# Kernel tuning notes

Hardware: AMD Instinct MI355X
Metric: run time of the kernel (lower is better)

The kernel has to match this reference:

```python
import jax, jax.numpy as jnp
import numpy as np

NUM_NODE = 5000
EMBED_DIM = 256
NUM_CLS = 20
EDGE_ROWS = (NUM_NODE - 1) * (NUM_NODE - 1) + 1  # 24990002
BZ, SEQ, NBR = 64, 512, 16


def setup_inputs() -> dict:
    key = jax.random.key(0)
    k = jax.random.split(key, 8)
    X = jax.random.randint(k[0], (BZ, SEQ), 0, NUM_NODE)
    NX = jax.random.randint(k[1], (BZ, SEQ, NBR), 0, NUM_NODE)
    EW = jax.random.randint(k[2], (BZ, SEQ, NBR), 0, EDGE_ROWS)
    # parameters (xavier-ish scale); padding_idx=0 rows zeroed
    node_emb = jax.random.normal(k[3], (NUM_NODE, EMBED_DIM), jnp.float32) * 0.02
    node_emb = node_emb.at[0].set(0.0)
    edge_w = jax.random.normal(k[4], (EDGE_ROWS, 1), jnp.float32) * 0.02
    edge_w = edge_w.at[0].set(0.0)
    node_w = jax.random.normal(k[5], (NUM_NODE, 1), jnp.float32) * 0.02
    node_w = node_w.at[0].set(0.0)
    fc_W = jax.random.normal(k[6], (NUM_CLS, EMBED_DIM), jnp.float32) * 0.05
    fc_b = jnp.zeros((NUM_CLS,), jnp.float32)
    return {"X": X, "NX": NX, "EW": EW, "node_emb": node_emb,
            "edge_w": edge_w, "node_w": node_w, "fc_W": fc_W, "fc_b": fc_b}


def reference(X, NX, EW, node_emb, edge_w, node_w, fc_W, fc_b):
    Ra = node_emb[NX]                      # (bz, seq, nbr, d) neighbor embeddings
    Ean = edge_w[EW]                       # (bz, seq, nbr, 1) edge weights
    Mn = jnp.max(Ra * Ean, axis=2)         # (bz, seq, d) max over neighbors
    Rn = node_emb[X]                       # (bz, seq, d)
    Nn = node_w[X]                         # (bz, seq, 1)
    y = (1.0 - Nn) * Mn + Nn * Rn          # weighted combine
    y = jnp.sum(y, axis=1)                 # (bz, d) sum-pool over sequence
    y = y @ fc_W.T + fc_b                  # (bz, num_cls)
    y = jax.nn.relu(y)
    # Dropout is identity at inference; LogSoftmax over dim=1
    return jax.nn.log_softmax(y, axis=1)
```

## Files before the change

### kernel.cpp

```cpp
#include <hip/hip_runtime.h>
#include <math.h>

#define NUM_NODE 5000
#define BZ   64
#define SEQ  512
#define NBR  16
#define DIM  256
#define NCLS 20

#define ROWB  (DIM * 2)
#define NCHUNK2 (SEQ / 4)
#define NCHUNK16 (SEQ / 16)

__device__ __forceinline__ int bcast_i(int v, int lane) {
    return __builtin_amdgcn_readlane(v, lane);
}
__device__ __forceinline__ float bcast_f(float v, int lane) {
    return __int_as_float(__builtin_amdgcn_readlane(__float_as_int(v), lane));
}
__device__ __forceinline__ unsigned bf16_rne(float f) {
    unsigned u = __float_as_uint(f);
    return (u + 0x7fffu + ((u >> 16) & 1u)) >> 16;
}
__device__ __forceinline__ float lo_bf16(unsigned u) { return __uint_as_float(u << 16); }
__device__ __forceinline__ float hi_bf16(unsigned u) { return __uint_as_float(u & 0xffff0000u); }

__global__ __launch_bounds__(256) void zero_ws_kernel(float* __restrict__ ws, int n) {
    int i = blockIdx.x * blockDim.x + threadIdx.x;
    if (i < n) ws[i] = 0.0f;
}

__global__ __launch_bounds__(256) void cvt_emb_zero_kernel(
    const float4* __restrict__ src, uint2* __restrict__ dst, int n4,
    float* __restrict__ ypre, int nacc) {
    int i = blockIdx.x * blockDim.x + threadIdx.x;
    if (i < n4) {
        float4 v = src[i];
        uint2 o;
        o.x = bf16_rne(v.x) | (bf16_rne(v.y) << 16);
        o.y = bf16_rne(v.z) | (bf16_rne(v.w) << 16);
        dst[i] = o;
    }
    if (i < nacc) ypre[i] = 0.0f;
}

__global__ __launch_bounds__(256, 8) void gnn_gather_kernel(
    const int*   __restrict__ X,
    const int*   __restrict__ NX,
    const int*   __restrict__ EW,
    const char*  __restrict__ embb,
    const float* __restrict__ edge_w,
    const float* __restrict__ node_w,
    float*       __restrict__ ypre)
{
    __shared__ float lds[4][DIM];

    const int b     = blockIdx.x / NCHUNK2;
    const int chunk = blockIdx.x % NCHUNK2;
    const int wave  = threadIdx.x >> 6;
    const int lane  = threadIdx.x & 63;
    const int half  = lane >> 5;
    const int sub   = lane & 31;
    const int voff  = sub * 16;

    const int s  = chunk * 4 + wave;
    const int bs = b * SEQ + s;

    int   nxv = 0;
    float ewv = 0.f;
    if (lane < NBR) {
        nxv = __builtin_nontemporal_load(&NX[bs * NBR + lane]);
        const int ewi = __builtin_nontemporal_load(&EW[bs * NBR + lane]);
        ewv = __builtin_nontemporal_load(&edge_w[ewi]);
    }
    const int   x  = X[bs];
    const float nn = node_w[x];

    uint4 e[8];
    #pragma unroll
    for (int j = 0; j < 8; ++j) {
        const int n0 = bcast_i(nxv, 2 * j);
        const int n1 = bcast_i(nxv, 2 * j + 1);
        const int n  = half ? n1 : n0;
        e[j] = *(const uint4*)(embb + (size_t)n * ROWB + voff);
    }
    const uint4 es = *(const uint4*)(embb + (size_t)x * ROWB + voff);

    float m[8];
    #pragma unroll
    for (int i = 0; i < 8; ++i) m[i] = -INFINITY;

    #pragma unroll
    for (int j = 0; j < 8; ++j) {
        const float w0 = bcast_f(ewv, 2 * j);
        const float w1 = bcast_f(ewv, 2 * j + 1);
        const float w  = half ? w1 : w0;
        m[0] = fmaxf(m[0], lo_bf16(e[j].x) * w);
        m[1] = fmaxf(m[1], hi_bf16(e[j].x) * w);
        m[2] = fmaxf(m[2], lo_bf16(e[j].y) * w);
        m[3] = fmaxf(m[3], hi_bf16(e[j].y) * w);
        m[4] = fmaxf(m[4], lo_bf16(e[j].z) * w);
        m[5] = fmaxf(m[5], hi_bf16(e[j].z) * w);
        m[6] = fmaxf(m[6], lo_bf16(e[j].w) * w);
        m[7] = fmaxf(m[7], hi_bf16(e[j].w) * w);
    }

    #pragma unroll
    for (int i = 0; i < 8; ++i)
        m[i] = fmaxf(m[i], __shfl_xor(m[i], 32));

    const float om = 1.0f - nn;
    float acc[8];
    acc[0] = om * m[0] + nn * lo_bf16(es.x);
    acc[1] = om * m[1] + nn * hi_bf16(es.x);
    acc[2] = om * m[2] + nn * lo_bf16(es.y);
    acc[3] = om * m[3] + nn * hi_bf16(es.y);
    acc[4] = om * m[4] + nn * lo_bf16(es.z);
    acc[5] = om * m[5] + nn * hi_bf16(es.z);
    acc[6] = om * m[6] + nn * lo_bf16(es.w);
    acc[7] = om * m[7] + nn * hi_bf16(es.w);

    if (half == 0) {
        *(float4*)&lds[wave][8 * sub]     = make_float4(acc[0], acc[1], acc[2], acc[3]);
        *(float4*)&lds[wave][8 * sub + 4] = make_float4(acc[4], acc[5], acc[6], acc[7]);
    }
    __syncthreads();

    const int t = threadIdx.x;
    atomicAdd(&ypre[b * DIM + t], lds[0][t] + lds[1][t] + lds[2][t] + lds[3][t]);
}

__global__ __launch_bounds__(256) void gnn_gather_f32_kernel(
    const int*   __restrict__ X,
    const int*   __restrict__ NX,
    const int*   __restrict__ EW,
    const float* __restrict__ node_emb,
    const float* __restrict__ edge_w,
    const float* __restrict__ node_w,
    float*       __restrict__ dst)
{
    __shared__ float lds[4][DIM];
    const int b     = blockIdx.x / NCHUNK16;
    const int chunk = blockIdx.x % NCHUNK16;
    const int wave  = threadIdx.x >> 6;
    const int lane  = threadIdx.x & 63;
    const int s0  = chunk * 16 + wave * 4;
    const int bs0 = b * SEQ + s0;

    const int   nx  = NX[bs0 * NBR + lane];
    const float ew  = edge_w[EW[bs0 * NBR + lane]];
    int xv = 0; float nwv = 0.f;
    if (lane < 4) { xv = X[bs0 + lane]; nwv = node_w[xv]; }

    float4 acc = make_float4(0.f, 0.f, 0.f, 0.f);
    for (int p = 0; p < 4; ++p) {
        float4 m = make_float4(-INFINITY, -INFINITY, -INFINITY, -INFINITY);
        for (int k = 0; k < NBR; ++k) {
            const int   n = bcast_i(nx, p * 16 + k);
            const float w = bcast_f(ew, p * 16 + k);
            const float4 e = *(const float4*)(node_emb + (size_t)n * DIM + 4 * lane);
            m.x = fmaxf(m.x, e.x * w); m.y = fmaxf(m.y, e.y * w);
            m.z = fmaxf(m.z, e.z * w); m.w = fmaxf(m.w, e.w * w);
        }
        const int   x  = bcast_i(xv, p);
        const float nn = bcast_f(nwv, p);
        const float om = 1.0f - nn;
        const float4 r = *(const float4*)(node_emb + (size_t)x * DIM + 4 * lane);
        acc.x += om * m.x + nn * r.x; acc.y += om * m.y + nn * r.y;
        acc.z += om * m.z + nn * r.z; acc.w += om * m.w + nn * r.w;
    }
    *(float4*)&lds[wave][4 * lane] = acc;
    __syncthreads();
    const int t = threadIdx.x;
    atomicAdd(&dst[b * DIM + t], lds[0][t] + lds[1][t] + lds[2][t] + lds[3][t]);
}

__global__ __launch_bounds__(256) void gnn_head_kernel(
    const float* __restrict__ ypre,
    const float* __restrict__ fc_W,
    const float* __restrict__ fc_b,
    float*       __restrict__ out)
{
    __shared__ float vals[NCLS];
    __shared__ float lse;

    const int b = blockIdx.x;
    const int t = threadIdx.x;
    const int wave = t >> 6;
    const int lane = t & 63;

    const float4 y4 = *(const float4*)(ypre + b * DIM + 4 * lane);

    #pragma unroll
    for (int ci = 0; ci < 5; ++ci) {
        const int c = wave * 5 + ci;
        const float4 w4 = *(const float4*)(fc_W + c * DIM + 4 * lane);
        float d = y4.x * w4.x + y4.y * w4.y + y4.z * w4.z + y4.w * w4.w;
        #pragma unroll
        for (int off = 32; off; off >>= 1) d += __shfl_xor(d, off);
        if (lane == 0) vals[c] = fmaxf(d + fc_b[c], 0.0f);
    }
    __syncthreads();

    if (t == 0) {
        float mx = -INFINITY;
        for (int c = 0; c < NCLS; ++c) mx = fmaxf(mx, vals[c]);
        float s = 0.0f;
        for (int c = 0; c < NCLS; ++c) s += expf(vals[c] - mx);
        lse = mx + logf(s);
    }
    __syncthreads();

    if (t < NCLS) out[b * NCLS + t] = vals[t] - lse;
}

extern "C" void kernel_launch(void* const* d_in, const int* in_sizes, int n_in,
                              void* d_out, int out_size, void* d_ws, size_t ws_size,
                              hipStream_t stream) {
    const int*   X        = (const int*)  d_in[0];
    const int*   NX       = (const int*)  d_in[1];
    const int*   EW       = (const int*)  d_in[2];
    const float* node_emb = (const float*)d_in[3];
    const float* edge_w   = (const float*)d_in[4];
    const float* node_w   = (const float*)d_in[5];
    const float* fc_W     = (const float*)d_in[6];
    const float* fc_b     = (const float*)d_in[7];
    float* out = (float*)d_out;

    const size_t acc_bytes = (size_t)BZ * DIM * sizeof(float);
    const size_t emb_bytes = (size_t)NUM_NODE * DIM * sizeof(unsigned short);
    float* ypre = (float*)d_ws;
    char*  embb = (char*)d_ws + acc_bytes;

    if (ws_size >= acc_bytes + emb_bytes) {
        const int n4 = NUM_NODE * DIM / 4;
        cvt_emb_zero_kernel<<<(n4 + 255) / 256, 256, 0, stream>>>(
            (const float4*)node_emb, (uint2*)embb, n4, ypre, BZ * DIM);
        gnn_gather_kernel<<<BZ * NCHUNK2, 256, 0, stream>>>(
            X, NX, EW, embb, edge_w, node_w, ypre);
        gnn_head_kernel<<<BZ, 256, 0, stream>>>(ypre, fc_W, fc_b, out);
    } else {
        zero_ws_kernel<<<(BZ * DIM + 255) / 256, 256, 0, stream>>>(ypre, BZ * DIM);
        gnn_gather_f32_kernel<<<BZ * NCHUNK16, 256, 0, stream>>>(
            X, NX, EW, node_emb, edge_w, node_w, ypre);
        gnn_head_kernel<<<BZ, 256, 0, stream>>>(ypre, fc_W, fc_b, out);
    }
}
```

Baseline: 176.4 us.

## Process eight positions per wave with double-buffered neighbor embedding loads

Each wave now handles eight sequence positions instead of one, accumulating them in registers, so the grid shrinks eightfold and there are far fewer LDS reductions and global atomics. Embedding gathers for the next position are issued into a second register buffer while the current one is reduced, overlapping memory latency with compute. The cost is a higher register count, with the occupancy hint lowered from 8 to 4 blocks, and fewer blocks in flight to hide the latency of the random gathers.

Result: slower. 199.4 us (+13.1%).

```diff
diff --git a/kernel.cpp b/kernel.cpp
--- a/kernel.cpp
+++ b/kernel.cpp
@@ -9,7 +9,9 @@
 #define NCLS 20
 
 #define ROWB  (DIM * 2)
-#define NCHUNK2 (SEQ / 4)
+#define PWAVE 8
+#define PBLK  32
+#define NCHUNKP (SEQ / PBLK)
 #define NCHUNK16 (SEQ / 16)
 
 __device__ __forceinline__ int bcast_i(int v, int lane) {
@@ -44,7 +46,7 @@
     if (i < nacc) ypre[i] = 0.0f;
 }
 
-__global__ __launch_bounds__(256, 8) void gnn_gather_kernel(
+__global__ __launch_bounds__(256, 4) void gnn_gather_kernel(
     const int*   __restrict__ X,
     const int*   __restrict__ NX,
     const int*   __restrict__ EW,
@@ -55,70 +57,92 @@
 {
     __shared__ float lds[4][DIM];
 
-    const int b     = blockIdx.x / NCHUNK2;
-    const int chunk = blockIdx.x % NCHUNK2;
+    const int b     = blockIdx.x / NCHUNKP;
+    const int chunk = blockIdx.x % NCHUNKP;
     const int wave  = threadIdx.x >> 6;
     const int lane  = threadIdx.x & 63;
     const int half  = lane >> 5;
     const int sub   = lane & 31;
     const int voff  = sub * 16;
 
-    const int s  = chunk * 4 + wave;
-    const int bs = b * SEQ + s;
-
-    int   nxv = 0;
-    float ewv = 0.f;
-    if (lane < NBR) {
-        nxv = __builtin_nontemporal_load(&NX[bs * NBR + lane]);
-        const int ewi = __builtin_nontemporal_load(&EW[bs * NBR + lane]);
-        ewv = __builtin_nontemporal_load(&edge_w[ewi]);
-    }
-    const int   x  = X[bs];
-    const float nn = node_w[x];
-
-    uint4 e[8];
+    const int s0  = chunk * PBLK + wave * PWAVE;
+    const int bs0 = b * SEQ + s0;
+
+    const int nxv0 = __builtin_nontemporal_load(&NX[bs0 * NBR + lane]);
+    const int nxv1 = __builtin_nontemporal_load(&NX[bs0 * NBR + 64 + lane]);
+    const int ewi0 = __builtin_nontemporal_load(&EW[bs0 * NBR + lane]);
+    const int ewi1 = __builtin_nontemporal_load(&EW[bs0 * NBR + 64 + lane]);
+    const float ewf0 = __builtin_nontemporal_load(&edge_w[ewi0]);
+    const float ewf1 = __builtin_nontemporal_load(&edge_w[ewi1]);
+
+    int xv = 0; float nwv = 0.f;
+    if (lane < PWAVE) {
+        xv  = __builtin_nontemporal_load(&X[bs0 + lane]);
+        nwv = node_w[xv];
+    }
+
+    float acc[8];
     #pragma unroll
-    for (int j = 0; j < 8; ++j) {
-        const int n0 = bcast_i(nxv, 2 * j);
-        const int n1 = bcast_i(nxv, 2 * j + 1);
-        const int n  = half ? n1 : n0;
-        e[j] = *(const uint4*)(embb + (size_t)n * ROWB + voff);
-    }
-    const uint4 es = *(const uint4*)(embb + (size_t)x * ROWB + voff);
-
-    float m[8];
+    for (int i = 0; i < 8; ++i) acc[i] = 0.f;
+
+    uint4 eA[8], eB[8], sA, sB;
+
+    auto issue = [&](int p, uint4 (&e)[8], uint4& es) {
+        const int nxr = (p < 4) ? nxv0 : nxv1;
+        const int lb  = (p & 3) * 16;
+        #pragma unroll
+        for (int j = 0; j < 8; ++j) {
+            const int n0 = bcast_i(nxr, lb + 2 * j);
+            const int n1 = bcast_i(nxr, lb + 2 * j + 1);
+            const int n  = half ? n1 : n0;
+            e[j] = *(const uint4*)(embb + (size_t)n * ROWB + voff);
+        }
+        es = *(const uint4*)(embb + (size_t)bcast_i(xv, p) * ROWB + voff);
+    };
+
+    auto consume = [&](int p, uint4 (&e)[8], uint4& es) {
+        const float ewr = (p < 4) ? ewf0 : ewf1;
+        const int   lb  = (p & 3) * 16;
+        float m[8];
+        #pragma unroll
+        for (int i = 0; i < 8; ++i) m[i] = -INFINITY;
+        #pragma unroll
+        for (int j = 0; j < 8; ++j) {
+            const float w0 = bcast_f(ewr, lb + 2 * j);
+            const float w1 = bcast_f(ewr, lb + 2 * j + 1);
+            const float w  = half ? w1 : w0;
+            m[0] = fmaxf(m[0], lo_bf16(e[j].x) * w);
+            m[1] = fmaxf(m[1], hi_bf16(e[j].x) * w);
+            m[2] = fmaxf(m[2], lo_bf16(e[j].y) * w);
+            m[3] = fmaxf(m[3], hi_bf16(e[j].y) * w);
+            m[4] = fmaxf(m[4], lo_bf16(e[j].z) * w);
+            m[5] = fmaxf(m[5], hi_bf16(e[j].z) * w);
+            m[6] = fmaxf(m[6], lo_bf16(e[j].w) * w);
+            m[7] = fmaxf(m[7], hi_bf16(e[j].w) * w);
+        }
+        #pragma unroll
+        for (int i = 0; i < 8; ++i)
+            m[i] = fmaxf(m[i], __shfl_xor(m[i], 32));
+        const float nn = bcast_f(nwv, p);
+        const float om = 1.0f - nn;
+        acc[0] += om * m[0] + nn * lo_bf16(es.x);
+        acc[1] += om * m[1] + nn * hi_bf16(es.x);
+        acc[2] += om * m[2] + nn * lo_bf16(es.y);
+        acc[3] += om * m[3] + nn * hi_bf16(es.y);
+        acc[4] += om * m[4] + nn * lo_bf16(es.z);
+        acc[5] += om * m[5] + nn * hi_bf16(es.z);
+        acc[6] += om * m[6] + nn * lo_bf16(es.w);
+        acc[7] += om * m[7] + nn * hi_bf16(es.w);
+    };
+
+    issue(0, eA, sA);
     #pragma unroll
-    for (int i = 0; i < 8; ++i) m[i] = -INFINITY;
-
-    #pragma unroll
-    for (int j = 0; j < 8; ++j) {
-        const float w0 = bcast_f(ewv, 2 * j);
-        const float w1 = bcast_f(ewv, 2 * j + 1);
-        const float w  = half ? w1 : w0;
-        m[0] = fmaxf(m[0], lo_bf16(e[j].x) * w);
-        m[1] = fmaxf(m[1], hi_bf16(e[j].x) * w);
-        m[2] = fmaxf(m[2], lo_bf16(e[j].y) * w);
-        m[3] = fmaxf(m[3], hi_bf16(e[j].y) * w);
-        m[4] = fmaxf(m[4], lo_bf16(e[j].z) * w);
-        m[5] = fmaxf(m[5], hi_bf16(e[j].z) * w);
-        m[6] = fmaxf(m[6], lo_bf16(e[j].w) * w);
-        m[7] = fmaxf(m[7], hi_bf16(e[j].w) * w);
-    }
-
-    #pragma unroll
-    for (int i = 0; i < 8; ++i)
-        m[i] = fmaxf(m[i], __shfl_xor(m[i], 32));
-
-    const float om = 1.0f - nn;
-    float acc[8];
-    acc[0] = om * m[0] + nn * lo_bf16(es.x);
-    acc[1] = om * m[1] + nn * hi_bf16(es.x);
-    acc[2] = om * m[2] + nn * lo_bf16(es.y);
-    acc[3] = om * m[3] + nn * hi_bf16(es.y);
-    acc[4] = om * m[4] + nn * lo_bf16(es.z);
-    acc[5] = om * m[5] + nn * hi_bf16(es.z);
-    acc[6] = om * m[6] + nn * lo_bf16(es.w);
-    acc[7] = om * m[7] + nn * hi_bf16(es.w);
+    for (int pp = 0; pp < 4; ++pp) {
+        issue(2 * pp + 1, eB, sB);
+        consume(2 * pp, eA, sA);
+        if (pp < 3) issue(2 * pp + 2, eA, sA);
+        consume(2 * pp + 1, eB, sB);
+    }
 
     if (half == 0) {
         *(float4*)&lds[wave][8 * sub]     = make_float4(acc[0], acc[1], acc[2], acc[3]);
@@ -236,7 +260,7 @@
         const int n4 = NUM_NODE * DIM / 4;
         cvt_emb_zero_kernel<<<(n4 + 255) / 256, 256, 0, stream>>>(
             (const float4*)node_emb, (uint2*)embb, n4, ypre, BZ * DIM);
-        gnn_gather_kernel<<<BZ * NCHUNK2, 256, 0, stream>>>(
+        gnn_gather_kernel<<<BZ * NCHUNKP, 256, 0, stream>>>(
             X, NX, EW, embb, edge_w, node_w, ypre);
         gnn_head_kernel<<<BZ, 256, 0, stream>>>(ypre, fc_W, fc_b, out);
     } else {
```

## Pre-gather edge weights in a separate pass and widen gather blocks to eight waves

Applied to the files above, without the earlier changes.

Adds a pre-pass kernel that gathers all edge weights from the large edge table into a dense workspace buffer, fused with the bf16 embedding conversion and the accumulator zeroing. The main gather kernel then reads the weights contiguously, which removes the dependent random load from its critical path. Its blocks grow to 512 threads covering 8 sequence positions, halving the number of atomics per output. The cost is an extra 2 MB write and read of the weight buffer, more workspace, and a larger block size that may affect occupancy.

Result: no change. 177.7 us (+0.7%).

```diff
diff --git a/kernel.cpp b/kernel.cpp
--- a/kernel.cpp
+++ b/kernel.cpp
@@ -8,8 +8,12 @@
 #define DIM  256
 #define NCLS 20
 
-#define ROWB  (DIM * 2)
-#define NCHUNK2 (SEQ / 4)
+#define ROWB    (DIM * 2)
+#define EDGE_N  (BZ * SEQ * NBR)
+#define EDGE_BLKS (EDGE_N / 256)
+#define CVT_N4  (NUM_NODE * DIM / 4)
+#define CVT_BLKS ((CVT_N4 + 255) / 256)
+#define CW      8
 #define NCHUNK16 (SEQ / 16)
 
 __device__ __forceinline__ int bcast_i(int v, int lane) {
@@ -30,48 +34,59 @@
     if (i < n) ws[i] = 0.0f;
 }
 
-__global__ __launch_bounds__(256) void cvt_emb_zero_kernel(
-    const float4* __restrict__ src, uint2* __restrict__ dst, int n4,
-    float* __restrict__ ypre, int nacc) {
-    int i = blockIdx.x * blockDim.x + threadIdx.x;
-    if (i < n4) {
-        float4 v = src[i];
-        uint2 o;
-        o.x = bf16_rne(v.x) | (bf16_rne(v.y) << 16);
-        o.y = bf16_rne(v.z) | (bf16_rne(v.w) << 16);
-        dst[i] = o;
-    }
-    if (i < nacc) ypre[i] = 0.0f;
-}
-
-__global__ __launch_bounds__(256, 8) void gnn_gather_kernel(
+__global__ __launch_bounds__(256) void pre_kernel(
+    const int*    __restrict__ EW,
+    const float*  __restrict__ edge_w,
+    float*        __restrict__ wbuf,
+    const float4* __restrict__ emb_src,
+    uint2*        __restrict__ embb_dst,
+    float*        __restrict__ ypre)
+{
+    const int blk = blockIdx.x;
+    const int t   = threadIdx.x;
+    if (blk < EDGE_BLKS) {
+        const int i   = blk * 256 + t;
+        const int idx = __builtin_nontemporal_load(&EW[i]);
+        wbuf[i] = __builtin_nontemporal_load(&edge_w[idx]);
+    } else {
+        const int i = (blk - EDGE_BLKS) * 256 + t;
+        if (i < CVT_N4) {
+            float4 v = emb_src[i];
+            uint2 o;
+            o.x = bf16_rne(v.x) | (bf16_rne(v.y) << 16);
+            o.y = bf16_rne(v.z) | (bf16_rne(v.w) << 16);
+            embb_dst[i] = o;
+        }
+        if (i < BZ * DIM) ypre[i] = 0.0f;
+    }
+}
+
+__global__ __launch_bounds__(512, 8) void gnn_gather_kernel(
     const int*   __restrict__ X,
     const int*   __restrict__ NX,
-    const int*   __restrict__ EW,
+    const float* __restrict__ wbuf,
     const char*  __restrict__ embb,
-    const float* __restrict__ edge_w,
     const float* __restrict__ node_w,
     float*       __restrict__ ypre)
 {
-    __shared__ float lds[4][DIM];
-
-    const int b     = blockIdx.x / NCHUNK2;
-    const int chunk = blockIdx.x % NCHUNK2;
+    __shared__ float lds[CW][DIM];
+
+    const int b     = blockIdx.x / (SEQ / CW);
+    const int chunk = blockIdx.x % (SEQ / CW);
     const int wave  = threadIdx.x >> 6;
     const int lane  = threadIdx.x & 63;
     const int half  = lane >> 5;
     const int sub   = lane & 31;
     const int voff  = sub * 16;
 
-    const int s  = chunk * 4 + wave;
+    const int s  = chunk * CW + wave;
     const int bs = b * SEQ + s;
 
     int   nxv = 0;
     float ewv = 0.f;
     if (lane < NBR) {
         nxv = __builtin_nontemporal_load(&NX[bs * NBR + lane]);
-        const int ewi = __builtin_nontemporal_load(&EW[bs * NBR + lane]);
-        ewv = __builtin_nontemporal_load(&edge_w[ewi]);
+        ewv = wbuf[bs * NBR + lane];
     }
     const int   x  = X[bs];
     const float nn = node_w[x];
@@ -126,8 +141,12 @@
     }
     __syncthreads();
 
-    const int t = threadIdx.x;
-    atomicAdd(&ypre[b * DIM + t], lds[0][t] + lds[1][t] + lds[2][t] + lds[3][t]);
+    if (threadIdx.x < DIM) {
+        float ssum = 0.f;
+        #pragma unroll
+        for (int w2 = 0; w2 < CW; ++w2) ssum += lds[w2][threadIdx.x];
+        atomicAdd(&ypre[b * DIM + threadIdx.x], ssum);
+    }
 }
 
 __global__ __launch_bounds__(256) void gnn_gather_f32_kernel(
@@ -228,16 +247,17 @@
     float* out = (float*)d_out;
 
     const size_t acc_bytes = (size_t)BZ * DIM * sizeof(float);
+    const size_t w_bytes   = (size_t)EDGE_N * sizeof(float);
     const size_t emb_bytes = (size_t)NUM_NODE * DIM * sizeof(unsigned short);
     float* ypre = (float*)d_ws;
-    char*  embb = (char*)d_ws + acc_bytes;
-
-    if (ws_size >= acc_bytes + emb_bytes) {
-        const int n4 = NUM_NODE * DIM / 4;
-        cvt_emb_zero_kernel<<<(n4 + 255) / 256, 256, 0, stream>>>(
-            (const float4*)node_emb, (uint2*)embb, n4, ypre, BZ * DIM);
-        gnn_gather_kernel<<<BZ * NCHUNK2, 256, 0, stream>>>(
-            X, NX, EW, embb, edge_w, node_w, ypre);
+    float* wbuf = (float*)((char*)d_ws + acc_bytes);
+    char*  embb = (char*)d_ws + acc_bytes + w_bytes;
+
+    if (ws_size >= acc_bytes + w_bytes + emb_bytes) {
+        pre_kernel<<<EDGE_BLKS + CVT_BLKS, 256, 0, stream>>>(
+            EW, edge_w, wbuf, (const float4*)node_emb, (uint2*)embb, ypre);
+        gnn_gather_kernel<<<BZ * (SEQ / CW), 512, 0, stream>>>(
+            X, NX, wbuf, embb, node_w, ypre);
         gnn_head_kernel<<<BZ, 256, 0, stream>>>(ypre, fc_W, fc_b, out);
     } else {
         zero_ws_kernel<<<(BZ * DIM + 255) / 256, 256, 0, stream>>>(ypre, BZ * DIM);
```

## Replace atomic accumulation with per-chunk partial sums reduced in head kernel

Applied to the files above, without the earlier changes.

The gather kernel now uses 512-thread blocks covering 8 sequence positions. Instead of atomically adding into a zeroed accumulator, it writes a per-block partial sum to a workspace buffer, and the head kernel reduces those partials. This removes the atomic contention and the need to zero the accumulator, and reorders the index loads so the EW load is issued first. In exchange it adds partial-buffer writes and reads (64×64×256 floats) and needs a larger workspace.

After: 179.0 us. Within noise of the previous version (+1.5%).

```diff
diff --git a/kernel.cpp b/kernel.cpp
--- a/kernel.cpp
+++ b/kernel.cpp
@@ -8,8 +8,10 @@
 #define DIM  256
 #define NCLS 20
 
-#define ROWB  (DIM * 2)
-#define NCHUNK2 (SEQ / 4)
+#define ROWB    (DIM * 2)
+#define CW      8
+#define NCHUNK  (SEQ / CW)
+#define CVT_N4  (NUM_NODE * DIM / 4)
 #define NCHUNK16 (SEQ / 16)
 
 __device__ __forceinline__ int bcast_i(int v, int lane) {
@@ -30,9 +32,8 @@
     if (i < n) ws[i] = 0.0f;
 }
 
-__global__ __launch_bounds__(256) void cvt_emb_zero_kernel(
-    const float4* __restrict__ src, uint2* __restrict__ dst, int n4,
-    float* __restrict__ ypre, int nacc) {
+__global__ __launch_bounds__(256) void cvt_emb_kernel(
+    const float4* __restrict__ src, uint2* __restrict__ dst, int n4) {
     int i = blockIdx.x * blockDim.x + threadIdx.x;
     if (i < n4) {
         float4 v = src[i];
@@ -41,38 +42,39 @@
         o.y = bf16_rne(v.z) | (bf16_rne(v.w) << 16);
         dst[i] = o;
     }
-    if (i < nacc) ypre[i] = 0.0f;
-}
-
-__global__ __launch_bounds__(256, 8) void gnn_gather_kernel(
+}
+
+__global__ __launch_bounds__(512, 8) void gnn_gather_kernel(
     const int*   __restrict__ X,
     const int*   __restrict__ NX,
     const int*   __restrict__ EW,
     const char*  __restrict__ embb,
     const float* __restrict__ edge_w,
     const float* __restrict__ node_w,
-    float*       __restrict__ ypre)
+    float*       __restrict__ part)
 {
-    __shared__ float lds[4][DIM];
-
-    const int b     = blockIdx.x / NCHUNK2;
-    const int chunk = blockIdx.x % NCHUNK2;
+    __shared__ float lds[CW][DIM];
+
+    const int b     = blockIdx.x / NCHUNK;
+    const int chunk = blockIdx.x % NCHUNK;
     const int wave  = threadIdx.x >> 6;
     const int lane  = threadIdx.x & 63;
     const int half  = lane >> 5;
     const int sub   = lane & 31;
     const int voff  = sub * 16;
 
-    const int s  = chunk * 4 + wave;
+    const int s  = chunk * CW + wave;
     const int bs = b * SEQ + s;
 
-    int   nxv = 0;
+    int   ewi = 0, nxv = 0;
     float ewv = 0.f;
     if (lane < NBR) {
+        ewi = __builtin_nontemporal_load(&EW[bs * NBR + lane]);
         nxv = __builtin_nontemporal_load(&NX[bs * NBR + lane]);
-        const int ewi = __builtin_nontemporal_load(&EW[bs * NBR + lane]);
+    }
+    if (lane < NBR)
         ewv = __builtin_nontemporal_load(&edge_w[ewi]);
-    }
+
     const int   x  = X[bs];
     const float nn = node_w[x];
 
@@ -126,8 +128,12 @@
     }
     __syncthreads();
 
-    const int t = threadIdx.x;
-    atomicAdd(&ypre[b * DIM + t], lds[0][t] + lds[1][t] + lds[2][t] + lds[3][t]);
+    if (threadIdx.x < DIM) {
+        float ssum = 0.f;
+        #pragma unroll
+        for (int w2 = 0; w2 < CW; ++w2) ssum += lds[w2][threadIdx.x];
+        part[((size_t)b * NCHUNK + chunk) * DIM + threadIdx.x] = ssum;
+    }
 }
 
 __global__ __launch_bounds__(256) void gnn_gather_f32_kernel(
@@ -176,11 +182,13 @@
 }
 
 __global__ __launch_bounds__(256) void gnn_head_kernel(
-    const float* __restrict__ ypre,
+    const float* __restrict__ part,
+    const int                 nchunk,
     const float* __restrict__ fc_W,
     const float* __restrict__ fc_b,
     float*       __restrict__ out)
 {
+    __shared__ float4 lds4[4][64];
     __shared__ float vals[NCLS];
     __shared__ float lse;
 
@@ -189,7 +197,19 @@
     const int wave = t >> 6;
     const int lane = t & 63;
 
-    const float4 y4 = *(const float4*)(ypre + b * DIM + 4 * lane);
+    float4 y = make_float4(0.f, 0.f, 0.f, 0.f);
+    for (int c = wave; c < nchunk; c += 4) {
+        const float4 v = *(const float4*)(part + ((size_t)b * nchunk + c) * DIM + 4 * lane);
+        y.x += v.x; y.y += v.y; y.z += v.z; y.w += v.w;
+    }
+    lds4[wave][lane] = y;
+    __syncthreads();
+    const float4 a0 = lds4[0][lane], a1 = lds4[1][lane];
+    const float4 a2 = lds4[2][lane], a3 = lds4[3][lane];
+    const float4 y4 = make_float4(a0.x + a1.x + a2.x + a3.x,
+                                  a0.y + a1.y + a2.y + a3.y,
+                                  a0.z + a1.z + a2.z + a3.z,
+                                  a0.w + a1.w + a2.w + a3.w);
 
     #pragma unroll
     for (int ci = 0; ci < 5; ++ci) {
@@ -227,22 +247,21 @@
     const float* fc_b     = (const float*)d_in[7];
     float* out = (float*)d_out;
 
-    const size_t acc_bytes = (size_t)BZ * DIM * sizeof(float);
-    const size_t emb_bytes = (size_t)NUM_NODE * DIM * sizeof(unsigned short);
-    float* ypre = (float*)d_ws;
-    char*  embb = (char*)d_ws + acc_bytes;
-
-    if (ws_size >= acc_bytes + emb_bytes) {
-        const int n4 = NUM_NODE * DIM / 4;
-        cvt_emb_zero_kernel<<<(n4 + 255) / 256, 256, 0, stream>>>(
-            (const float4*)node_emb, (uint2*)embb, n4, ypre, BZ * DIM);
-        gnn_gather_kernel<<<BZ * NCHUNK2, 256, 0, stream>>>(
-            X, NX, EW, embb, edge_w, node_w, ypre);
-        gnn_head_kernel<<<BZ, 256, 0, stream>>>(ypre, fc_W, fc_b, out);
+    const size_t part_bytes = (size_t)BZ * NCHUNK * DIM * sizeof(float);
+    const size_t emb_bytes  = (size_t)NUM_NODE * DIM * sizeof(unsigned short);
+    float* part = (float*)d_ws;
+    char*  embb = (char*)d_ws + part_bytes;
+
+    if (ws_size >= part_bytes + emb_bytes) {
+        cvt_emb_kernel<<<(CVT_N4 + 255) / 256, 256, 0, stream>>>(
+            (const float4*)node_emb, (uint2*)embb, CVT_N4);
+        gnn_gather_kernel<<<BZ * NCHUNK, 512, 0, stream>>>(
+            X, NX, EW, embb, edge_w, node_w, part);
+        gnn_head_kernel<<<BZ, 256, 0, stream>>>(part, NCHUNK, fc_W, fc_b, out);
     } else {
-        zero_ws_kernel<<<(BZ * DIM + 255) / 256, 256, 0, stream>>>(ypre, BZ * DIM);
+        zero_ws_kernel<<<(BZ * DIM + 255) / 256, 256, 0, stream>>>(part, BZ * DIM);
         gnn_gather_f32_kernel<<<BZ * NCHUNK16, 256, 0, stream>>>(
-            X, NX, EW, node_emb, edge_w, node_w, ypre);
-        gnn_head_kernel<<<BZ, 256, 0, stream>>>(ypre, fc_W, fc_b, out);
-    }
-}
+            X, NX, EW, node_emb, edge_w, node_w, part);
+        gnn_head_kernel<<<BZ, 256, 0, stream>>>(part, 1, fc_W, fc_b, out);
+    }
+}
```
